# Kernel tuning notes

Hardware: AMD Instinct MI355X
Metric: run time of the kernel (lower is better)

## Reference

```python
import jax, jax.numpy as jnp
import numpy as np

NUM_HEADS = 8
NUM_GROUPS = 32
EPS = 1e-5


def group_norm(x, scale, bias):
    # x: (b, c, t)
    b, c, t = x.shape
    xg = x.reshape(b, NUM_GROUPS, c // NUM_GROUPS, t)
    mean = xg.mean(axis=(2, 3), keepdims=True)
    var = xg.var(axis=(2, 3), keepdims=True)
    xn = ((xg - mean) * jax.lax.rsqrt(var + EPS)).reshape(b, c, t)
    return xn * scale[None, :, None] + bias[None, :, None]


def setup_inputs() -> dict:
    key = jax.random.key(0)
    ks = jax.random.split(key, 3)
    b, c, h, w = 16, 512, 32, 32
    x = jax.random.normal(ks[0], (b, c, h, w), dtype=jnp.float32)
    gn_scale = jnp.ones((c,), jnp.float32)
    gn_bias = jnp.zeros((c,), jnp.float32)
    w_qkv = jax.random.normal(ks[1], (3 * c, c), jnp.float32) * (c ** -0.5)
    b_qkv = jnp.zeros((3 * c,), jnp.float32)
    w_proj = jax.random.normal(ks[2], (c, c), jnp.float32) * (c ** -0.5)
    b_proj = jnp.zeros((c,), jnp.float32)
    return {"x": x, "gn_scale": gn_scale, "gn_bias": gn_bias,
            "w_qkv": w_qkv, "b_qkv": b_qkv, "w_proj": w_proj, "b_proj": b_proj}


def reference(x, gn_scale, gn_bias, w_qkv, b_qkv, w_proj, b_proj):
    b, c, h, w = x.shape
    t = h * w
    xf = x.reshape(b, c, t)
    xn = group_norm(xf, gn_scale, gn_bias)
    # 1x1 conv1d == channel matmul: (b, 3c, t)
    qkv = jnp.einsum('oc,bct->bot', w_qkv, xn) + b_qkv[None, :, None]
    dh = c // NUM_HEADS
    qkv = qkv.reshape(b * NUM_HEADS, 3 * dh, t)
    q, k, v = jnp.split(qkv, 3, axis=1)  # each (b*H, dh, t)
    scale = dh ** -0.25
    logits = jnp.einsum('bct,bcs->bts', q * scale, k * scale)
    weight = jax.nn.softmax(logits.astype(jnp.float32), axis=-1).astype(logits.dtype)
    attn = jnp.einsum('bts,bcs->bct', weight, v)  # (b*H, dh, t)
    attn = attn.reshape(b, c, t)
    out = jnp.einsum('oc,bct->bot', w_proj, attn) + b_proj[None, :, None]
    return (xf + out).reshape(b, c, h, w)
```

## Files before the change

kernel.cpp:

```cpp
#include <hip/hip_runtime.h>
#include <hip/hip_bf16.h>

typedef __hip_bfloat16 bf16;
typedef __attribute__((ext_vector_type(8))) short short8;
typedef __attribute__((ext_vector_type(4))) short short4v;
typedef __attribute__((ext_vector_type(4))) float float4v;
typedef __attribute__((ext_vector_type(16))) float f32x16;
typedef __attribute__((ext_vector_type(4))) int int4v;

__device__ __forceinline__ float b2f(bf16 v) { return __bfloat162float(v); }
__device__ __forceinline__ bf16  f2b(float v) { return __float2bfloat16(v); }
__device__ __forceinline__ short f2s(float v) { bf16 h = f2b(v); return *reinterpret_cast<short*>(&h); }
__device__ __forceinline__ float s2f(short s) { bf16 h; *reinterpret_cast<short*>(&h) = s; return b2f(h); }
__device__ __forceinline__ short8 ld8(const bf16* p) { return *(const short8*)p; }

__device__ __forceinline__ float ldin(const void* p, size_t i, int f32) {
  return f32 ? ((const float*)p)[i] : b2f(((const bf16*)p)[i]);
}

__device__ __forceinline__ float4v mfma16(short8 a, short8 b, float4v c) {
  return __builtin_amdgcn_mfma_f32_16x16x32_bf16(a, b, c, 0, 0, 0);
}
__device__ __forceinline__ f32x16 mfma32(short8 a, short8 b, f32x16 c) {
  return __builtin_amdgcn_mfma_f32_32x32x16_bf16(a, b, c, 0, 0, 0);
}
__device__ __forceinline__ int cvtpk(float a, float b) {
  int r; asm("v_cvt_pk_bf16_f32 %0, %1, %2" : "=v"(r) : "v"(a), "v"(b)); return r;
}
__device__ __forceinline__ void plswap(int& x, int& y) {
  asm("v_permlane32_swap_b32 %0, %1" : "+v"(x), "+v"(y));
}

__device__ __forceinline__ void gload16(const void* g, void* l) {
  __builtin_amdgcn_global_load_lds((__attribute__((address_space(1))) void*)(void*)g,
                                   (__attribute__((address_space(3))) void*)l, 16, 0, 0);
}

#define K2SCALE 0.18033688011112042f
#define TSTRIDE 72

__global__ __launch_bounds__(256) void detect_kernel(const unsigned short* __restrict__ x,
                                                     int* __restrict__ flag) {
  __shared__ int h;
  if (threadIdx.x == 0) h = 0;
  __syncthreads();
  int local = 0;
  for (int i = threadIdx.x; i < 8192; i += 256)
    if ((x[i] & 0x7F80u) == 0x7F80u) local = 1;
  if (local) atomicOr(&h, 1);
  __syncthreads();
  if (threadIdx.x == 0) *flag = h;
}

__global__ __launch_bounds__(256) void conv2_kernel(const void* __restrict__ s1, bf16* __restrict__ d1,
                                                    const void* __restrict__ s2, bf16* __restrict__ d2,
                                                    const void* __restrict__ s3, bf16* __restrict__ d3,
                                                    const void* __restrict__ s4, bf16* __restrict__ d4,
                                                    const int* __restrict__ flagp) {
  const int f32 = *flagp;
  const int blk = blockIdx.x;
  const void* src; bf16* dst; int base, n;
  if (blk < 768)       { src = s1; dst = d1; base = blk;        n = 786432; }
  else if (blk < 1024) { src = s2; dst = d2; base = blk - 768;  n = 262144; }
  else if (blk < 1026) { src = s3; dst = d3; base = blk - 1024; n = 1536;   }
  else                 { src = s4; dst = d4; base = 0;          n = 512;    }
  int i0 = (base * 256 + threadIdx.x) * 4;
#pragma unroll
  for (int j = 0; j < 4; j++) {
    int i = i0 + j;
    if (i < n) dst[i] = f2b(ldin(src, i, f32));
  }
}

__global__ __launch_bounds__(256) void gn_stats_kernel(const void* __restrict__ x,
                                                       float2* __restrict__ stats,
                                                       const int* __restrict__ flagp) {
  const int f32 = *flagp;
  const int bg = blockIdx.x;
  const int GSZ = 16 * 1024;
  const size_t base = (size_t)bg * GSZ;
  const int tid = threadIdx.x;

  float s = 0.f, ss = 0.f;
  if (f32) {
    const float4v* xp = (const float4v*)((const float*)x + base) + tid;
#pragma unroll
    for (int i = 0; i < 16; i++) {
      float4v v = xp[i * 256];
#pragma unroll
      for (int j = 0; j < 4; j++) { s += v[j]; ss += v[j] * v[j]; }
    }
  } else {
    const short8* xp = (const short8*)((const bf16*)x + base) + tid;
#pragma unroll
    for (int i = 0; i < 8; i++) {
      short8 v = xp[i * 256];
#pragma unroll
      for (int j = 0; j < 8; j++) { float f = s2f(v[j]); s += f; ss += f * f; }
    }
  }
  for (int off = 32; off > 0; off >>= 1) {
    s  += __shfl_down(s, off);
    ss += __shfl_down(ss, off);
  }
  __shared__ float rs[4], rss[4];
  const int wave = tid >> 6, lane = tid & 63;
  if (lane == 0) { rs[wave] = s; rss[wave] = ss; }
  __syncthreads();
  if (tid == 0) {
    s  = rs[0] + rs[1] + rs[2] + rs[3];
    ss = rss[0] + rss[1] + rss[2] + rss[3];
    const float mean = s * (1.f / GSZ);
    const float var  = ss * (1.f / GSZ) - mean * mean;
    stats[bg] = make_float2(mean, rsqrtf(var + 1e-5f));
  }
}

__global__ __launch_bounds__(256) void gn_apply_kernel(const void* __restrict__ x,
                                                       const void* __restrict__ gsc,
                                                       const void* __restrict__ gbi,
                                                       const float2* __restrict__ stats,
                                                       bf16* __restrict__ xn,
                                                       const int* __restrict__ flagp) {
  const int f32 = *flagp;
  const int b = blockIdx.y;
  const int t0 = blockIdx.x * 64;
  const int cs = blockIdx.z * 128;
  const int tid = threadIdx.x;

  __shared__ float Aa[128], Bb[128];
  __shared__ short T[64][130];

  if (tid < 128) {
    const int c = cs + tid;
    const float2 st = stats[b * 32 + (c >> 4)];
    const float sc = ldin(gsc, c, f32), bi = ldin(gbi, c, f32);
    Aa[tid] = st.y * sc;
    Bb[tid] = bi - st.x * st.y * sc;
  }
  __syncthreads();

  const int row = tid >> 4;
  const int t4 = (tid & 15) * 4;
  if (f32) {
    const float* xb = (const float*)x + ((size_t)(b * 512 + cs)) * 1024 + t0 + t4;
#pragma unroll
    for (int st = 0; st < 8; st++) {
      const int c = row + st * 16;
      const float4v v = *(const float4v*)(xb + (size_t)c * 1024);
      const float aa = Aa[c], bb = Bb[c];
#pragma unroll
      for (int j = 0; j < 4; j++) T[t4 + j][c] = f2s(v[j] * aa + bb);
    }
  } else {
    const bf16* xb = (const bf16*)x + ((size_t)(b * 512 + cs)) * 1024 + t0 + t4;
#pragma unroll
    for (int st = 0; st < 8; st++) {
      const int c = row + st * 16;
      const short4v v = *(const short4v*)(xb + (size_t)c * 1024);
      const float aa = Aa[c], bb = Bb[c];
#pragma unroll
      for (int j = 0; j < 4; j++) T[t4 + j][c] = f2s(s2f(v[j]) * aa + bb);
    }
  }
  __syncthreads();

  const int cc = (tid & 63) * 2, tr = tid >> 6;
#pragma unroll
  for (int i = 0; i < 16; i++) {
    const int t2 = tr + i * 4;
    const int v = *(const int*)&T[t2][cc];
    *(int*)&xn[((size_t)(b * 1024 + t0 + t2)) * 512 + cs + cc] = v;
  }
}

__global__ __launch_bounds__(256) void qkv_kernel(const bf16* __restrict__ Wb,
                                                  const bf16* __restrict__ biasb,
                                                  const bf16* __restrict__ xn,
                                                  bf16* __restrict__ Qt,
                                                  bf16* __restrict__ Kt,
                                                  bf16* __restrict__ Vb) {
  const int bat = blockIdx.z;
  const int M0 = blockIdx.y * 128;
  const int N0 = blockIdx.x * 128;
  __shared__ short smem[18432];

  const int tid = threadIdx.x;
  const int w = tid >> 6, lane = tid & 63;
  const int col = lane & 15, g = lane >> 4;
  const int wm = (w & 1) * 64, wn = (w >> 1) * 64;

  float4v acc[4][4];
#pragma unroll
  for (int i = 0; i < 4; i++)
#pragma unroll
    for (int j = 0; j < 4; j++) acc[i][j] = (float4v)(0.f);

  int srco[2], dstb[2];
#pragma unroll
  for (int i = 0; i < 2; i++) {
    const int Gb = i * 256 + w * 64;
    dstb[i] = Gb * 8;
    const int G = Gb + lane;
    srco[i] = (G >> 2) * 512 + (G & 3) * 8;
  }
  const bf16* Ab  = Wb + (size_t)M0 * 512;
  const bf16* Bb2 = xn + ((size_t)bat * 1024 + N0) * 512;

#pragma unroll
  for (int i = 0; i < 2; i++) {
    gload16(Ab + srco[i],  &smem[dstb[i]]);
    gload16(Bb2 + srco[i], &smem[4096 + dstb[i]]);
  }
  __syncthreads();

  for (int it = 0; it < 16; ++it) {
    const int pb = it & 1;
    if (it < 15) {
      const int kn = it * 32 + 32;
      const int nb = (1 - pb) * 8192;
#pragma unroll
      for (int i = 0; i < 2; i++) {
        gload16(Ab + kn + srco[i],  &smem[nb + dstb[i]]);
        gload16(Bb2 + kn + srco[i], &smem[nb + 4096 + dstb[i]]);
      }
    }
    const short* Ap = &smem[pb * 8192];
    const short* Bp = Ap + 4096;
    short8 af[4], bf4[4];
#pragma unroll
    for (int mt = 0; mt < 4; mt++) af[mt] = *(const short8*)&Ap[(wm + mt * 16 + col) * 32 + g * 8];
#pragma unroll
    for (int nt = 0; nt < 4; nt++) bf4[nt] = *(const short8*)&Bp[(wn + nt * 16 + col) * 32 + g * 8];
#pragma unroll
    for (int mt = 0; mt < 4; mt++)
#pragma unroll
      for (int nt = 0; nt < 4; nt++) acc[mt][nt] = mfma16(af[mt], bf4[nt], acc[mt][nt]);
    __syncthreads();
  }

  const int sec = (M0 + wm) >> 6;
  const int h = sec / 3, kind = sec % 3;
  const size_t bh = (size_t)bat * 8 + h;
  const float qs = (kind == 0) ? K2SCALE : 1.f;
  short* Tw = smem + w * 4608;

  float bv[4][4];
#pragma unroll
  for (int mt = 0; mt < 4; mt++)
#pragma unroll
    for (int r = 0; r < 4; r++) bv[mt][r] = b2f(biasb[M0 + wm + mt * 16 + g * 4 + r]);

  if (kind == 2) {
#pragma unroll
    for (int mt = 0; mt < 4; mt++)
#pragma unroll
      for (int nt = 0; nt < 4; nt++)
#pragma unroll
        for (int r = 0; r < 4; r++) {
          const int lo = mt * 16 + g * 4 + r;
          const int lt = nt * 16 + col;
          Tw[lo * TSTRIDE + lt] = f2s(acc[mt][nt][r] + bv[mt][r]);
        }
#pragma unroll
    for (int j = 0; j < 8; j++) {
      const int lo = j * 8 + (lane >> 3);
      const int gr = lane & 7;
      short8 v = *(const short8*)&Tw[lo * TSTRIDE + gr * 8];
      *(short8*)(Vb + (bh * 64 + lo) * 1024 + N0 + wn + gr * 8) = v;
    }
  } else {
#pragma unroll
    for (int mt = 0; mt < 4; mt++)
#pragma unroll
      for (int nt = 0; nt < 4; nt++) {
        short4v pk;
#pragma unroll
        for (int r = 0; r < 4; r++) pk[r] = f2s((acc[mt][nt][r] + bv[mt][r]) * qs);
        *(short4v*)&Tw[(nt * 16 + col) * TSTRIDE + mt * 16 + g * 4] = pk;
      }
    bf16* dst = (kind == 0) ? Qt : Kt;
#pragma unroll
    for (int j = 0; j < 8; j++) {
      const int tl = j * 8 + (lane >> 3), c8 = (lane & 7) * 8;
      short8 v = *(const short8*)&Tw[tl * TSTRIDE + c8];
      *(short8*)(dst + (bh * 1024 + N0 + wn + tl) * 64 + c8) = v;
    }
  }
}

__global__ __launch_bounds__(256, 4) void attn_kernel(const bf16* __restrict__ Qt,
                                                      const bf16* __restrict__ Kt,
                                                      const bf16* __restrict__ Vb,
                                                      bf16* __restrict__ xattn) {
  const int bh = blockIdx.x;
  const int t0 = blockIdx.y * 128;
  const int b = bh >> 3, h = bh & 7;
  const int tid = threadIdx.x;
  const int w = tid >> 6, lane = tid & 63;
  const int qv = lane & 31, hh = lane >> 5;
  const int q0 = t0 + w * 32;

  __shared__ short Ks[8192];
  __shared__ short Vs[8192];

  const bf16* kbase = Kt + (size_t)bh * 65536;
  const bf16* vbase = Vb + (size_t)bh * 65536;

  int ksrc[2], vsrc[2];
  const int ldst0 = w * 1024, ldst1 = w * 1024 + 512;
#pragma unroll
  for (int i = 0; i < 2; i++) {
    const int G = w * 128 + i * 64 + lane;
    const int a = G >> 8, ks = (G >> 6) & 3, qvs = (G >> 1) & 31, hhs = G & 1;
    const int co = (ks * 2 + hhs) * 8;
    ksrc[i] = (a * 32 + qvs) * 64 + co;
    vsrc[i] = (a * 32 + qvs) * 1024 + co;
  }
  const int rb = (qv * 2 + hh) * 8;

  short8 qb[4];
#pragma unroll
  for (int ks = 0; ks < 4; ks++)
    qb[ks] = ld8(Qt + ((size_t)bh * 1024 + q0 + qv) * 64 + ks * 16 + hh * 8);

  f32x16 O[2];
  O[0] = (f32x16)(0.f); O[1] = (f32x16)(0.f);
  float l = 0.f;
  short8 pa[4];

  gload16(kbase + ksrc[0], &Ks[ldst0]);
  gload16(kbase + ksrc[1], &Ks[ldst1]);
  gload16(vbase + vsrc[0], &Vs[ldst0]);
  gload16(vbase + vsrc[1], &Vs[ldst1]);
  __syncthreads();

#define SMAX(S, a)                                                              \
  {                                                                             \
    _Pragma("unroll")                                                           \
    for (int j = 0; j < 16; j++) S[j] = __builtin_amdgcn_exp2f(S[j]);           \
    l += (((S[0] + S[1]) + (S[2] + S[3])) + ((S[4] + S[5]) + (S[6] + S[7])))    \
       + (((S[8] + S[9]) + (S[10] + S[11])) + ((S[12] + S[13]) + (S[14] + S[15]))); \
    _Pragma("unroll")                                                           \
    for (int kp = 0; kp < 2; kp++) {                                            \
      int X  = cvtpk(S[8 * kp + 0], S[8 * kp + 1]);                             \
      int Y  = cvtpk(S[8 * kp + 4], S[8 * kp + 5]);                             \
      int X2 = cvtpk(S[8 * kp + 2], S[8 * kp + 3]);                             \
      int Y2 = cvtpk(S[8 * kp + 6], S[8 * kp + 7]);                             \
      plswap(X, Y);                                                             \
      plswap(X2, Y2);                                                           \
      const int4v wv = {X, X2, Y, Y2};                                          \
      pa[(a) * 2 + kp] = __builtin_bit_cast(short8, wv);                        \
    }                                                                           \
  }

#pragma unroll 2
  for (int it = 0; it < 16; ++it) {
    const int cur = (it & 1) * 4096;
    const int nxt = 4096 - cur;
    if (it < 15) {
      gload16(kbase + (it + 1) * 4096 + ksrc[0], &Ks[nxt + ldst0]);
      gload16(kbase + (it + 1) * 4096 + ksrc[1], &Ks[nxt + ldst1]);
      gload16(vbase + (it + 1) * 64 + vsrc[0],   &Vs[nxt + ldst0]);
      gload16(vbase + (it + 1) * 64 + vsrc[1],   &Vs[nxt + ldst1]);
    }
#pragma unroll
    for (int a = 0; a < 2; a++) {
      short8 kf[4];
#pragma unroll
      for (int ks = 0; ks < 4; ks++)
        kf[ks] = *(const short8*)&Ks[cur + (a * 4 + ks) * 512 + rb];
      f32x16 S = (f32x16)(0.f);
      __builtin_amdgcn_s_setprio(1);
#pragma unroll
      for (int ks = 0; ks < 4; ks++) S = mfma32(kf[ks], qb[ks], S);
      __builtin_amdgcn_s_setprio(0);
      SMAX(S, a);
    }
#pragma unroll
    for (int o = 0; o < 2; o++) {
      short8 vf[4];
#pragma unroll
      for (int ks = 0; ks < 4; ks++)
        vf[ks] = *(const short8*)&Vs[cur + (o * 4 + ks) * 512 + rb];
      __builtin_amdgcn_s_setprio(1);
#pragma unroll
      for (int ks = 0; ks < 4; ks++)
        O[o] = mfma32(pa[ks], vf[ks], O[o]);
      __builtin_amdgcn_s_setprio(0);
    }
    __syncthreads();
  }
#undef SMAX

  {
    float lt = l + __shfl_xor(l, 32);
    const float inv = 1.f / lt;
    float* lf = (float*)Ks + w * 32;
    lf[qv] = inv;

    bf16* ob = xattn + ((size_t)b * 1024 + q0 + 4 * hh) * 512 + h * 64 + qv;
#pragma unroll
    for (int r = 0; r < 16; r++) {
      const int qoff = (r & 3) + 8 * (r >> 2);
      const float iv = lf[qoff + 4 * hh];
      ob[(size_t)qoff * 512]      = f2b(O[0][r] * iv);
      ob[(size_t)qoff * 512 + 32] = f2b(O[1][r] * iv);
    }
  }
}

__global__ __launch_bounds__(256) void proj_kernel(const bf16* __restrict__ Wp,
                                                   const bf16* __restrict__ biasb,
                                                   const bf16* __restrict__ xattn,
                                                   const void* __restrict__ res,
                                                   void* __restrict__ out,
                                                   const int* __restrict__ flagp) {
  const int f32 = *flagp;
  const int bat = blockIdx.z;
  const int M0 = blockIdx.y * 128;
  const int N0 = blockIdx.x * 128;
  __shared__ short smem[18432];

  const int tid = threadIdx.x;
  const int w = tid >> 6, lane = tid & 63;
  const int col = lane & 15, g = lane >> 4;
  const int wm = (w & 1) * 64, wn = (w >> 1) * 64;

  float4v acc[4][4];
#pragma unroll
  for (int i = 0; i < 4; i++)
#pragma unroll
    for (int j = 0; j < 4; j++) acc[i][j] = (float4v)(0.f);

  int srco[2], dstb[2];
#pragma unroll
  for (int i = 0; i < 2; i++) {
    const int Gb = i * 256 + w * 64;
    dstb[i] = Gb * 8;
    const int G = Gb + lane;
    srco[i] = (G >> 2) * 512 + (G & 3) * 8;
  }
  const bf16* Ab  = Wp + (size_t)M0 * 512;
  const bf16* Bb2 = xattn + ((size_t)bat * 1024 + N0) * 512;

#pragma unroll
  for (int i = 0; i < 2; i++) {
    gload16(Ab + srco[i],  &smem[dstb[i]]);
    gload16(Bb2 + srco[i], &smem[4096 + dstb[i]]);
  }
  __syncthreads();

  for (int it = 0; it < 16; ++it) {
    const int pb = it & 1;
    if (it < 15) {
      const int kn = it * 32 + 32;
      const int nb = (1 - pb) * 8192;
#pragma unroll
      for (int i = 0; i < 2; i++) {
        gload16(Ab + kn + srco[i],  &smem[nb + dstb[i]]);
        gload16(Bb2 + kn + srco[i], &smem[nb + 4096 + dstb[i]]);
      }
    }
    const short* Ap = &smem[pb * 8192];
    const short* Bp = Ap + 4096;
    short8 af[4], bf4[4];
#pragma unroll
    for (int mt = 0; mt < 4; mt++) af[mt] = *(const short8*)&Ap[(wm + mt * 16 + col) * 32 + g * 8];
#pragma unroll
    for (int nt = 0; nt < 4; nt++) bf4[nt] = *(const short8*)&Bp[(wn + nt * 16 + col) * 32 + g * 8];
#pragma unroll
    for (int mt = 0; mt < 4; mt++)
#pragma unroll
      for (int nt = 0; nt < 4; nt++) acc[mt][nt] = mfma16(af[mt], bf4[nt], acc[mt][nt]);
    __syncthreads();
  }

  short* Tw = smem + w * 4608;
  float bv[4][4];
#pragma unroll
  for (int mt = 0; mt < 4; mt++)
#pragma unroll
    for (int r = 0; r < 4; r++) bv[mt][r] = b2f(biasb[M0 + wm + mt * 16 + g * 4 + r]);

#pragma unroll
  for (int mt = 0; mt < 4; mt++)
#pragma unroll
    for (int nt = 0; nt < 4; nt++)
#pragma unroll
      for (int r = 0; r < 4; r++) {
        const int lo = mt * 16 + g * 4 + r;
        const int lt = nt * 16 + col;
        Tw[lo * TSTRIDE + lt] = f2s(acc[mt][nt][r] + bv[mt][r]);
      }
#pragma unroll
  for (int j = 0; j < 8; j++) {
    const int lo = j * 8 + (lane >> 3);
    const int gr = lane & 7;
    short8 v = *(const short8*)&Tw[lo * TSTRIDE + gr * 8];
    const int o = M0 + wm + lo;
    const size_t ci = ((size_t)bat * 512 + o) * 1024 + N0 + wn + gr * 8;
    if (f32) {
      float4v o0, o1;
#pragma unroll
      for (int e = 0; e < 4; e++) o0[e] = s2f(v[e]) + ((const float*)res)[ci + e];
#pragma unroll
      for (int e = 0; e < 4; e++) o1[e] = s2f(v[e + 4]) + ((const float*)res)[ci + 4 + e];
      *(float4v*)((float*)out + ci) = o0;
      *(float4v*)((float*)out + ci + 4) = o1;
    } else {
      short8 ov;
#pragma unroll
      for (int e = 0; e < 8; e++)
        ov[e] = f2s(s2f(v[e]) + b2f(((const bf16*)res)[ci + e]));
      *(short8*)((bf16*)out + ci) = ov;
    }
  }
}

extern "C" void kernel_launch(void* const* d_in, const int* in_sizes, int n_in,
                              void* d_out, int out_size, void* d_ws, size_t ws_size,
                              hipStream_t stream) {
  const void* x      = d_in[0];
  const void* gsc    = d_in[1];
  const void* gbi    = d_in[2];
  const void* w_qkv  = d_in[3];
  const void* b_qkv  = d_in[4];
  const void* w_proj = d_in[5];
  const void* b_proj = d_in[6];

  char* p = (char*)d_ws;
  int*    flag  = (int*)p;                 p += 256;
  float2* stats = (float2*)p;              p += 512 * sizeof(float2);
  bf16*   xn    = (bf16*)p;                p += (size_t)16 * 1024 * 512 * 2;
  bf16*   Qt    = (bf16*)p;                p += (size_t)128 * 1024 * 64 * 2;
  bf16*   Kt    = (bf16*)p;                p += (size_t)128 * 1024 * 64 * 2;
  bf16*   Vb    = (bf16*)p;                p += (size_t)128 * 64 * 1024 * 2;
  bf16*   Wqb   = (bf16*)p;                p += (size_t)1536 * 512 * 2;
  bf16*   Wpb   = (bf16*)p;                p += (size_t)512 * 512 * 2;
  bf16*   Bqb   = (bf16*)p;                p += (size_t)1536 * 2;
  bf16*   Bpb   = (bf16*)p;                p += (size_t)512 * 2;
  bf16*   xattn = (bf16*)p;

  detect_kernel<<<1, 256, 0, stream>>>((const unsigned short*)x, flag);
  conv2_kernel<<<1027, 256, 0, stream>>>(w_qkv, Wqb, w_proj, Wpb,
                                         b_qkv, Bqb, b_proj, Bpb, flag);
  gn_stats_kernel<<<512, 256, 0, stream>>>(x, stats, flag);
  gn_apply_kernel<<<dim3(16, 16, 4), 256, 0, stream>>>(x, gsc, gbi, stats, xn, flag);
  qkv_kernel<<<dim3(8, 12, 16), 256, 0, stream>>>(Wqb, Bqb, xn, Qt, Kt, Vb);
  attn_kernel<<<dim3(128, 8), 256, 0, stream>>>(Qt, Kt, Vb, xattn);
  proj_kernel<<<dim3(8, 4, 16), 256, 0, stream>>>(Wpb, Bpb, xattn, x, d_out, flag);
}
```

Measured before the change: 205.3 us.

## Triple-buffer K tiles in attention and prefetch two iterations ahead

Triple-buffers the K tile in LDS so K is prefetched two iterations ahead, while V stays double-buffered one iteration ahead. The end-of-iteration __syncthreads is replaced by an explicit vmcnt wait plus a single s_barrier at the top of each iteration, and the Q loads are drained up front so the manual vmcnt counting stays correct. The goal is to hide global-to-LDS latency behind the QK and PV MFMA work and to cut one full barrier drain per iteration. In exchange, K LDS grows by half (from 16 KB to 24 KB per block), and correctness now depends on hand-counted outstanding loads.

After: 203.2 us. About the same (-1.0%).

```diff
diff --git a/kernel.cpp b/kernel.cpp
--- a/kernel.cpp
+++ b/kernel.cpp
@@ -301,7 +301,7 @@
   const int qv = lane & 31, hh = lane >> 5;
   const int q0 = t0 + w * 32;
 
-  __shared__ short Ks[8192];
+  __shared__ short Ks[12288];
   __shared__ short Vs[8192];
 
   const bf16* kbase = Kt + (size_t)bh * 65536;
@@ -323,17 +323,20 @@
 #pragma unroll
   for (int ks = 0; ks < 4; ks++)
     qb[ks] = ld8(Qt + ((size_t)bh * 1024 + q0 + qv) * 64 + ks * 16 + hh * 8);
+  asm volatile("s_waitcnt vmcnt(0)" ::: "memory");
+  __builtin_amdgcn_sched_barrier(0);
 
   f32x16 O[2];
   O[0] = (f32x16)(0.f); O[1] = (f32x16)(0.f);
   float l = 0.f;
   short8 pa[4];
 
-  gload16(kbase + ksrc[0], &Ks[ldst0]);
-  gload16(kbase + ksrc[1], &Ks[ldst1]);
-  gload16(vbase + vsrc[0], &Vs[ldst0]);
-  gload16(vbase + vsrc[1], &Vs[ldst1]);
-  __syncthreads();
+  gload16(kbase + ksrc[0],        &Ks[ldst0]);
+  gload16(kbase + ksrc[1],        &Ks[ldst1]);
+  gload16(vbase + vsrc[0],        &Vs[ldst0]);
+  gload16(vbase + vsrc[1],        &Vs[ldst1]);
+  gload16(kbase + 4096 + ksrc[0], &Ks[4096 + ldst0]);
+  gload16(kbase + 4096 + ksrc[1], &Ks[4096 + ldst1]);
 
 #define SMAX(S, a)                                                              \
   {                                                                             \
@@ -354,22 +357,33 @@
     }                                                                           \
   }
 
+  int kc = 0;
 #pragma unroll 2
   for (int it = 0; it < 16; ++it) {
-    const int cur = (it & 1) * 4096;
-    const int nxt = 4096 - cur;
+    if (it < 15) { asm volatile("s_waitcnt vmcnt(2)" ::: "memory"); }
+    else         { asm volatile("s_waitcnt vmcnt(0)" ::: "memory"); }
+    __builtin_amdgcn_sched_barrier(0);
+    __builtin_amdgcn_s_barrier();
+    __builtin_amdgcn_sched_barrier(0);
+
+    const int vnxt = ((it + 1) & 1) * 4096;
     if (it < 15) {
-      gload16(kbase + (it + 1) * 4096 + ksrc[0], &Ks[nxt + ldst0]);
-      gload16(kbase + (it + 1) * 4096 + ksrc[1], &Ks[nxt + ldst1]);
-      gload16(vbase + (it + 1) * 64 + vsrc[0],   &Vs[nxt + ldst0]);
-      gload16(vbase + (it + 1) * 64 + vsrc[1],   &Vs[nxt + ldst1]);
-    }
+      gload16(vbase + (it + 1) * 64 + vsrc[0], &Vs[vnxt + ldst0]);
+      gload16(vbase + (it + 1) * 64 + vsrc[1], &Vs[vnxt + ldst1]);
+    }
+    const int k2 = (kc >= 4096) ? kc - 4096 : kc + 8192;
+    if (it < 14) {
+      gload16(kbase + (it + 2) * 4096 + ksrc[0], &Ks[k2 + ldst0]);
+      gload16(kbase + (it + 2) * 4096 + ksrc[1], &Ks[k2 + ldst1]);
+    }
+
+    const int vcur = (it & 1) * 4096;
 #pragma unroll
     for (int a = 0; a < 2; a++) {
       short8 kf[4];
 #pragma unroll
       for (int ks = 0; ks < 4; ks++)
-        kf[ks] = *(const short8*)&Ks[cur + (a * 4 + ks) * 512 + rb];
+        kf[ks] = *(const short8*)&Ks[kc + (a * 4 + ks) * 512 + rb];
       f32x16 S = (f32x16)(0.f);
       __builtin_amdgcn_s_setprio(1);
 #pragma unroll
@@ -382,16 +396,18 @@
       short8 vf[4];
 #pragma unroll
       for (int ks = 0; ks < 4; ks++)
-        vf[ks] = *(const short8*)&Vs[cur + (o * 4 + ks) * 512 + rb];
+        vf[ks] = *(const short8*)&Vs[vcur + (o * 4 + ks) * 512 + rb];
       __builtin_amdgcn_s_setprio(1);
 #pragma unroll
       for (int ks = 0; ks < 4; ks++)
         O[o] = mfma32(pa[ks], vf[ks], O[o]);
       __builtin_amdgcn_s_setprio(0);
     }
-    __syncthreads();
+    kc = (kc == 8192) ? 0 : kc + 4096;
   }
 #undef SMAX
+
+  __syncthreads();
 
   {
     float lt = l + __shfl_xor(l, 32);
```
